# Optimization experiments

Measured on AMD Instinct MI355X. Metric: run time of the kernel, lower is better.

The kernel has to match this reference:

```python
import jax, jax.numpy as jnp
import numpy as np

VOCAB = 49408
D = 768
H = 12
DH = D // H
FF = 3072
L = 4
B = 32
S = 512
EPS = 1e-6


def _pos_encoding(seq_len, d):
    pos = np.arange(seq_len, dtype=np.float64)[:, None]
    j = np.arange(d, dtype=np.float64)[None, :]
    ang = pos / np.power(10000.0, 2.0 * (j // 2) / d)
    pe = np.where((np.arange(d) % 2) == 0, np.sin(ang), np.cos(ang))
    return jnp.asarray(pe, dtype=jnp.float32)  # [seq_len, d]


def _layernorm(x, g, b):
    m = jnp.mean(x, axis=-1, keepdims=True)
    v = jnp.mean(jnp.square(x - m), axis=-1, keepdims=True)
    return g * (x - m) * jax.lax.rsqrt(v + EPS) + b


def setup_inputs() -> dict:
    key = jax.random.key(0)
    ks = jax.random.split(key, 16)
    s = 0.02
    inp = {
        "tokens": jax.random.randint(ks[0], (B, S), 0, VOCAB, dtype=jnp.int32),
        "emb": jax.random.normal(ks[1], (VOCAB, D), jnp.float32) * s,
        "wq": jax.random.normal(ks[2], (L, D, D), jnp.float32) * s,
        "bq": jnp.zeros((L, D), jnp.float32),
        "wk": jax.random.normal(ks[3], (L, D, D), jnp.float32) * s,
        "bk": jnp.zeros((L, D), jnp.float32),
        "wv": jax.random.normal(ks[4], (L, D, D), jnp.float32) * s,
        "bv": jnp.zeros((L, D), jnp.float32),
        "wo": jax.random.normal(ks[5], (L, D, D), jnp.float32) * s,
        "bo": jnp.zeros((L, D), jnp.float32),
        "w1": jax.random.normal(ks[6], (L, D, FF), jnp.float32) * s,
        "b1": jnp.zeros((L, FF), jnp.float32),
        "w2": jax.random.normal(ks[7], (L, FF, D), jnp.float32) * s,
        "b2": jnp.zeros((L, D), jnp.float32),
        "ln1_g": jnp.ones((L, D), jnp.float32),
        "ln1_b": jnp.zeros((L, D), jnp.float32),
        "ln2_g": jnp.ones((L, D), jnp.float32),
        "ln2_b": jnp.zeros((L, D), jnp.float32),
        "wl": jax.random.normal(ks[8], (D, 32), jnp.float32) * s,
        "bl": jnp.zeros((32,), jnp.float32),
        "wout": jax.random.normal(ks[9], (32, 1), jnp.float32) * s,
        "bout": jnp.zeros((1,), jnp.float32),
    }
    return inp


def reference(tokens, emb, wq, bq, wk, bk, wv, bv, wo, bo, w1, b1, w2, b2,
              ln1_g, ln1_b, ln2_g, ln2_b, wl, bl, wout, bout):
    seq_len = tokens.shape[1]
    pe = _pos_encoding(seq_len, D)  # [S, D] constant
    x = emb[tokens] * jnp.sqrt(jnp.float32(D)) + pe[None, :, :]  # [B,S,D]
    scale = 1.0 / jnp.sqrt(jnp.float32(DH))
    for i in range(L):
        # multi-head attention (naive full score matrix, mask=None)
        q = (jnp.einsum('bsd,de->bse', x, wq[i]) + bq[i]).reshape(-1, seq_len, H, DH)
        k = (jnp.einsum('bsd,de->bse', x, wk[i]) + bk[i]).reshape(-1, seq_len, H, DH)
        v = (jnp.einsum('bsd,de->bse', x, wv[i]) + bv[i]).reshape(-1, seq_len, H, DH)
        scores = jnp.einsum('bqhd,bkhd->bhqk', q, k) * scale  # [B,H,S,S]
        attn = jax.nn.softmax(scores, axis=-1)
        av = jnp.einsum('bhqk,bkhd->bqhd', attn, v).reshape(-1, seq_len, D)
        attn_out = jnp.einsum('bsd,de->bse', av, wo[i]) + bo[i]
        out1 = _layernorm(x + attn_out, ln1_g[i], ln1_b[i])
        # FFN: relu -> dense
        h = jax.nn.relu(jnp.einsum('bsd,df->bsf', out1, w1[i]) + b1[i])
        ffn = jnp.einsum('bsf,fd->bsd', h, w2[i]) + b2[i]
        x = _layernorm(out1 + ffn, ln2_g[i], ln2_b[i])
    pooled = jnp.mean(x, axis=1)  # GlobalAveragePooling1D -> [B,D]
    h = jax.nn.gelu(pooled @ wl + bl, approximate=False)
    out = jax.nn.sigmoid(h @ wout + bout)  # [B,1]
    return out
```

## Files before the change

kernel.cpp:

```cpp
#include <hip/hip_runtime.h>
#include <hip/hip_bf16.h>
#include <math.h>


#define B_  32
#define S_  512
#define D_  768
#define H_  12
#define DH_ 64
#define FF_ 3072
#define L_  4
#define QKVSTR 2304

typedef __attribute__((ext_vector_type(8))) short short8;
typedef __attribute__((ext_vector_type(4))) short short4v;
typedef __attribute__((ext_vector_type(4))) float f32x4;

__device__ __forceinline__ void async16(const void* g, void* l) {
    __builtin_amdgcn_global_load_lds(
        (const __attribute__((address_space(1))) void*)g,
        (__attribute__((address_space(3))) void*)l, 16, 0, 0);
}

__device__ __forceinline__ ushort f2bf(float f) {
    __hip_bfloat16 h = __float2bfloat16(f);
    return __builtin_bit_cast(ushort, h);
}
__device__ __forceinline__ float bflo(uint u) { return __uint_as_float(u << 16); }
__device__ __forceinline__ float bfhi(uint u) { return __uint_as_float(u & 0xffff0000u); }

__device__ __forceinline__ short8 scale8_eighth(short8 v) {
    short8 r;
#pragma unroll
    for (int e = 0; e < 8; e++) {
        ushort u = (ushort)v[e];
        ushort ex = u & 0x7f80;
        r[e] = (short)(ex > 0x0180 ? (ushort)(u - 0x0180) : (ushort)(u & 0x8000));
    }
    return r;
}

__global__ void pe_kernel(float* __restrict__ pe) {
    int idx = blockIdx.x * 256 + threadIdx.x;
    if (idx >= S_ * D_) return;
    int s = idx / D_, j = idx % D_;
    double e = (2.0 * (double)(j >> 1)) / (double)D_;
    double denom = pow(10000.0, e);
    double ang = (double)s / denom;
    pe[idx] = (j & 1) ? (float)cos(ang) : (float)sin(ang);
}

__global__ void embed_kernel(const int* __restrict__ tokens,
                             const float* __restrict__ emb,
                             const float* __restrict__ pe,
                             __hip_bfloat16* __restrict__ xb) {
    int row = blockIdx.x;
    int s = row & (S_ - 1);
    int tok = tokens[row];
    float scale = sqrtf((float)D_);
    for (int i = threadIdx.x; i < D_; i += 256) {
        float v = emb[(size_t)tok * D_ + i] * scale + pe[s * D_ + i];
        xb[(size_t)row * D_ + i] = __float2bfloat16(v);
    }
}

__global__ __launch_bounds__(256) void transpose_bf16_l(
    const float* __restrict__ in, __hip_bfloat16* __restrict__ out,
    int R, int C, size_t inL, size_t outL)
{
    __shared__ float tile[32][33];
    in  += (size_t)blockIdx.z * inL;
    out += (size_t)blockIdx.z * outL;
    int tx = threadIdx.x & 31, ty = threadIdx.x >> 5;
    int c0 = blockIdx.x * 32, r0 = blockIdx.y * 32;
#pragma unroll
    for (int d = 0; d < 32; d += 8)
        tile[ty + d][tx] = in[(size_t)(r0 + ty + d) * C + c0 + tx];
    __syncthreads();
#pragma unroll
    for (int d = 0; d < 32; d += 8)
        out[(size_t)(c0 + ty + d) * R + r0 + tx] = __float2bfloat16(tile[tx][ty + d]);
}

__global__ void biascat(const float* __restrict__ bq, const float* __restrict__ bk,
                        const float* __restrict__ bv, float* __restrict__ o) {
    int i = blockIdx.x * 256 + threadIdx.x;
    int ll = i / QKVSTR, j = i % QKVSTR;
    o[i] = j < 768 ? bq[ll * 768 + j]
         : j < 1536 ? bk[ll * 768 + j - 768]
                    : bv[ll * 768 + j - 1536];
}

#define BAR()   __builtin_amdgcn_s_barrier()
#define LGKM0() asm volatile("s_waitcnt lgkmcnt(0)" ::: "memory")
#define VM4()   asm volatile("s_waitcnt vmcnt(4)" ::: "memory")
#define VM0()   asm volatile("s_waitcnt vmcnt(0)" ::: "memory")

#define STAGE_A(buf, h, kt) do { \
    async16(aSrc[h][0] + (kt) * 64, &lds[(buf) * 2][dOff[h][0]]); \
    async16(aSrc[h][1] + (kt) * 64, &lds[(buf) * 2][dOff[h][1]]); } while (0)
#define STAGE_B(buf, h, kt) do { \
    async16(bSrc[h][0] + (kt) * 64, &lds[(buf) * 2 + 1][dOff[h][0]]); \
    async16(bSrc[h][1] + (kt) * 64, &lds[(buf) * 2 + 1][dOff[h][1]]); } while (0)

#define LDA(buf, m, ks) (*(const short8*)((const char*)(&lds[(buf) * 2][0]) + \
    (size_t)((arow + (m) * 16) * 128 + cswz[ks])))
#define LDB(buf, n, ks) (*(const short8*)((const char*)(&lds[(buf) * 2 + 1][0]) + \
    (size_t)((brow + (n) * 16) * 128 + cswz[ks])))

#define MFMA_Q(mh, nh) do { \
    __builtin_amdgcn_s_setprio(1); \
    _Pragma("unroll") \
    for (int ks_ = 0; ks_ < 2; ks_++) { \
      _Pragma("unroll") \
      for (int n_ = 0; n_ < 2; n_++) { \
        _Pragma("unroll") \
        for (int m_ = 0; m_ < 4; m_++) { \
          acc[(mh) * 4 + m_][(nh) * 2 + n_] = \
              __builtin_amdgcn_mfma_f32_16x16x32_bf16( \
                  a[m_][ks_], b[(nh) * 2 + n_][ks_], \
                  acc[(mh) * 4 + m_][(nh) * 2 + n_], 0, 0, 0); \
        } } } \
    __builtin_amdgcn_s_setprio(0); \
} while (0)

template<int RELU>
__global__ __launch_bounds__(512, 2) void gemm256(
    const ushort* __restrict__ A,
    const ushort* __restrict__ Bt,
    const float* __restrict__ bias,
    __hip_bfloat16* __restrict__ C,
    int M, int N, int K, int NX)
{
    __shared__ alignas(16) ushort lds[4][16384];

    int t = threadIdx.x;
    int l = t & 63, w = t >> 6;
    int wmi = w >> 2, wni = w & 3;
    int lm = l & 15, lo = l >> 4;

    int nwg = gridDim.x;
    int bid = blockIdx.x;
    int lid = (nwg & 7) ? bid : ((bid & 7) * (nwg >> 3) + (bid >> 3));
    int bn = lid % NX, bm = lid / NX;
    int row0 = bm << 8, col0 = bn << 8;

    const ushort* aSrc[2][2];
    const ushort* bSrc[2][2];
    int dOff[2][2];
#pragma unroll
    for (int h = 0; h < 2; h++) {
#pragma unroll
        for (int c = 0; c < 2; c++) {
            int p = h * 16384 + c * 8192 + t * 16;
            int prow = p >> 7;
            int scolb = (p & 127) ^ ((prow & 7) << 4);
            dOff[h][c] = p >> 1;
            aSrc[h][c] = A  + (size_t)(row0 + prow) * K + (scolb >> 1);
            bSrc[h][c] = Bt + (size_t)(col0 + prow) * K + (scolb >> 1);
        }
    }

    int arow = wmi * 128 + lm;
    int brow = wni * 64 + lm;
    int swz = (lm & 7) << 4;
    int cswz[2];
    cswz[0] = (lo * 16) ^ swz;
    cswz[1] = (64 + lo * 16) ^ swz;

    f32x4 acc[8][4];
#pragma unroll
    for (int i = 0; i < 8; i++)
#pragma unroll
        for (int j = 0; j < 4; j++) acc[i][j] = (f32x4){0.f, 0.f, 0.f, 0.f};
    short8 a[4][2], b[4][2];

    const int NK = K >> 6;
    const int NI = NK >> 1;

    STAGE_A(0, 0, 0); STAGE_A(0, 1, 0);
    STAGE_B(0, 0, 0); STAGE_B(0, 1, 0);
    STAGE_B(1, 0, 1); STAGE_B(1, 1, 1);
    VM4();
    BAR();

    for (int i = 0; i < NI; i++) {
        int kt  = 2 * i;
        int ktA = (kt + 2 <= NK - 2) ? kt + 2 : NK - 2;
        int ktB = (kt + 3 <= NK - 1) ? kt + 3 : NK - 1;

#pragma unroll
        for (int m = 0; m < 4; m++) { a[m][0] = LDA(0, m, 0); a[m][1] = LDA(0, m, 1); }
#pragma unroll
        for (int n = 0; n < 2; n++) { b[n][0] = LDB(0, n, 0); b[n][1] = LDB(0, n, 1); }
        STAGE_A(1, 0, kt + 1);
        BAR(); LGKM0();
        MFMA_Q(0, 0);
        BAR();

#pragma unroll
        for (int n = 0; n < 2; n++) { b[2 + n][0] = LDB(0, 2 + n, 0); b[2 + n][1] = LDB(0, 2 + n, 1); }
        STAGE_A(1, 1, kt + 1);
        BAR(); LGKM0();
        MFMA_Q(0, 1);
        BAR();

#pragma unroll
        for (int m = 0; m < 4; m++) { a[m][0] = LDA(0, 4 + m, 0); a[m][1] = LDA(0, 4 + m, 1); }
        STAGE_B(0, 0, ktA);
        BAR(); LGKM0();
        MFMA_Q(1, 0);
        BAR();

        STAGE_B(0, 1, ktA);
        BAR(); LGKM0();
        MFMA_Q(1, 1);
        VM4();
        BAR();

#pragma unroll
        for (int m = 0; m < 4; m++) { a[m][0] = LDA(1, m, 0); a[m][1] = LDA(1, m, 1); }
#pragma unroll
        for (int n = 0; n < 2; n++) { b[n][0] = LDB(1, n, 0); b[n][1] = LDB(1, n, 1); }
        STAGE_A(0, 0, ktA);
        BAR(); LGKM0();
        MFMA_Q(0, 0);
        BAR();

#pragma unroll
        for (int n = 0; n < 2; n++) { b[2 + n][0] = LDB(1, 2 + n, 0); b[2 + n][1] = LDB(1, 2 + n, 1); }
        STAGE_A(0, 1, ktA);
        BAR(); LGKM0();
        MFMA_Q(0, 1);
        BAR();

#pragma unroll
        for (int m = 0; m < 4; m++) { a[m][0] = LDA(1, 4 + m, 0); a[m][1] = LDA(1, 4 + m, 1); }
        STAGE_B(1, 0, ktB);
        BAR(); LGKM0();
        MFMA_Q(1, 0);
        BAR();

        STAGE_B(1, 1, ktB);
        BAR(); LGKM0();
        MFMA_Q(1, 1);
        VM4();
        BAR();
    }

    VM0();
    BAR();

    ushort* eL = &lds[0][0];
    {
        int crow = wmi * 128;
        int ccol = wni * 64;
#pragma unroll
        for (int n = 0; n < 4; n++) {
            int c = ccol + n * 16 + lm;
            float bs = bias[col0 + c];
#pragma unroll
            for (int m = 0; m < 8; m++) {
#pragma unroll
                for (int r = 0; r < 4; r++) {
                    float v = acc[m][n][r] + bs;
                    if (RELU) v = fmaxf(v, 0.f);
                    int row = crow + m * 16 + lo * 4 + r;
                    int sc = c ^ (((lo * 4 + r) & 7) << 3);
                    eL[row * 256 + sc] = f2bf(v);
                }
            }
        }
    }
    __syncthreads();
    {
        int rsw = ((t >> 5) & 7) << 3;
#pragma unroll
        for (int i = 0; i < 16; i++) {
            int byteoff = i * 8192 + t * 16;
            int rr = byteoff >> 9;
            int cc = (byteoff & 511) >> 1;
            uint4 v = *(const uint4*)(eL + rr * 256 + (cc ^ rsw));
            *(uint4*)(C + (size_t)(row0 + rr) * N + col0 + cc) = v;
        }
    }
    (void)M;
}

#define PSTR 72
__global__ __launch_bounds__(256) void attn_mfma(
    const ushort* __restrict__ qkv,
    __hip_bfloat16* __restrict__ av)
{
    __shared__ alignas(16) ushort sQP[128 * PSTR];
    __shared__ alignas(16) ushort sK[64 * PSTR];
    __shared__ alignas(16) ushort sVt[64 * PSTR];

    int t = threadIdx.x;
    int qt = blockIdx.x, h = blockIdx.y, b = blockIdx.z;
    int w = t >> 6, l = t & 63;
    int lm = l & 15, lq = l >> 4;
    int wm = w * 32;

    const ushort* qbase = qkv + (size_t)(b * S_ + qt * 128) * QKVSTR + h * DH_;
    const ushort* kbase = qkv + (size_t)b * S_ * QKVSTR + 768 + h * DH_;
    const ushort* vbase = qkv + (size_t)b * S_ * QKVSTR + 1536 + h * DH_;

    {
        int r = t >> 1, c0 = (t & 1) * 32;
        const ushort* src = qbase + (size_t)r * QKVSTR + c0;
        ushort* dst = &sQP[r * PSTR + c0];
        *(uint4*)(dst + 0)  = *(const uint4*)(src + 0);
        *(uint4*)(dst + 8)  = *(const uint4*)(src + 8);
        *(uint4*)(dst + 16) = *(const uint4*)(src + 16);
        *(uint4*)(dst + 24) = *(const uint4*)(src + 24);
    }
    __syncthreads();
    short8 qf[2][2];
#pragma unroll
    for (int i = 0; i < 2; i++)
#pragma unroll
        for (int ks = 0; ks < 2; ks++)
            qf[i][ks] = scale8_eighth(
                *(const short8*)&sQP[(wm + i * 16 + lm) * PSTR + ks * 32 + lq * 8]);

    ushort* sPw = &sQP[(size_t)wm * PSTR];

    f32x4 accO[4][2];
    float mrun[2], lrun[2];
#pragma unroll
    for (int dk = 0; dk < 4; dk++)
#pragma unroll
        for (int i = 0; i < 2; i++) accO[dk][i] = (f32x4){0.f, 0.f, 0.f, 0.f};
    mrun[0] = mrun[1] = -1e30f;
    lrun[0] = lrun[1] = 0.f;

    for (int kt = 0; kt < S_ / 64; kt++) {
        __syncthreads();
        {
            int r = t >> 2, c0 = (t & 3) * 16;
            const ushort* ksrc = kbase + (size_t)(kt * 64 + r) * QKVSTR + c0;
            ushort* kdst = &sK[r * PSTR + c0];
            *(uint4*)(kdst + 0) = *(const uint4*)(ksrc + 0);
            *(uint4*)(kdst + 8) = *(const uint4*)(ksrc + 8);
            int p = t & 31, d0 = (t >> 5) * 8;
            const ushort* vsrc = vbase + (size_t)(kt * 64 + 2 * p) * QKVSTR + d0;
            uint4 v0 = *(const uint4*)(vsrc);
            uint4 v1 = *(const uint4*)(vsrc + QKVSTR);
            const ushort* e0 = (const ushort*)&v0;
            const ushort* e1 = (const ushort*)&v1;
#pragma unroll
            for (int j = 0; j < 8; j++) {
                uint pk = (uint)e0[j] | ((uint)e1[j] << 16);
                *(uint*)&sVt[(d0 + j) * PSTR + 2 * p] = pk;
            }
        }
        __syncthreads();

        f32x4 accS[4][2];
#pragma unroll
        for (int sb = 0; sb < 4; sb++)
#pragma unroll
            for (int i = 0; i < 2; i++) accS[sb][i] = (f32x4){0.f, 0.f, 0.f, 0.f};
#pragma unroll
        for (int ks = 0; ks < 2; ks++) {
#pragma unroll
            for (int sb = 0; sb < 4; sb++) {
                short8 kf = *(const short8*)&sK[(sb * 16 + lm) * PSTR + ks * 32 + lq * 8];
#pragma unroll
                for (int i = 0; i < 2; i++)
                    accS[sb][i] = __builtin_amdgcn_mfma_f32_16x16x32_bf16(
                        kf, qf[i][ks], accS[sb][i], 0, 0, 0);
            }
        }

        float pmax[2];
#pragma unroll
        for (int i = 0; i < 2; i++) {
            float m0 = accS[0][i][0];
#pragma unroll
            for (int sb = 0; sb < 4; sb++)
#pragma unroll
                for (int r = 0; r < 4; r++) m0 = fmaxf(m0, accS[sb][i][r]);
            m0 = fmaxf(m0, __shfl_xor(m0, 16));
            m0 = fmaxf(m0, __shfl_xor(m0, 32));
            pmax[i] = m0;
        }
        float alpha[2];
#pragma unroll
        for (int i = 0; i < 2; i++) {
            float mn = fmaxf(mrun[i], pmax[i]);
            alpha[i] = __expf(mrun[i] - mn);
            mrun[i] = mn;
        }
        float rsum[2] = {0.f, 0.f};
#pragma unroll
        for (int sb = 0; sb < 4; sb++)
#pragma unroll
            for (int i = 0; i < 2; i++)
#pragma unroll
                for (int r = 0; r < 4; r++) {
                    float p = __expf(accS[sb][i][r] - mrun[i]);
                    accS[sb][i][r] = p;
                    rsum[i] += p;
                }
#pragma unroll
        for (int i = 0; i < 2; i++) {
            rsum[i] += __shfl_xor(rsum[i], 16);
            rsum[i] += __shfl_xor(rsum[i], 32);
            lrun[i] = lrun[i] * alpha[i] + rsum[i];
        }

#pragma unroll
        for (int dk = 0; dk < 4; dk++)
#pragma unroll
            for (int i = 0; i < 2; i++)
#pragma unroll
                for (int r = 0; r < 4; r++) accO[dk][i][r] *= alpha[i];

#pragma unroll
        for (int i = 0; i < 2; i++)
#pragma unroll
            for (int sb = 0; sb < 4; sb++) {
                short4v pk;
#pragma unroll
                for (int r = 0; r < 4; r++) pk[r] = (short)f2bf(accS[sb][i][r]);
                *(short4v*)&sPw[(i * 16 + lm) * PSTR + sb * 16 + lq * 4] = pk;
            }

#pragma unroll
        for (int ks = 0; ks < 2; ks++) {
            short8 pf[2];
#pragma unroll
            for (int i = 0; i < 2; i++)
                pf[i] = *(const short8*)&sPw[(i * 16 + lm) * PSTR + ks * 32 + lq * 8];
#pragma unroll
            for (int dk = 0; dk < 4; dk++) {
                short8 vf = *(const short8*)&sVt[(dk * 16 + lm) * PSTR + ks * 32 + lq * 8];
#pragma unroll
                for (int i = 0; i < 2; i++)
                    accO[dk][i] = __builtin_amdgcn_mfma_f32_16x16x32_bf16(
                        vf, pf[i], accO[dk][i], 0, 0, 0);
            }
        }
    }

    float invl[2];
    invl[0] = 1.0f / lrun[0];
    invl[1] = 1.0f / lrun[1];
#pragma unroll
    for (int i = 0; i < 2; i++) {
        int row = qt * 128 + wm + i * 16 + lm;
        __hip_bfloat16* dst = av + (size_t)(b * S_ + row) * D_ + h * DH_;
#pragma unroll
        for (int dk = 0; dk < 4; dk++) {
            short4v ok;
#pragma unroll
            for (int r = 0; r < 4; r++) ok[r] = (short)f2bf(accO[dk][i][r] * invl[i]);
            *(short4v*)(dst + dk * 16 + lq * 4) = ok;
        }
    }
}

__global__ __launch_bounds__(256) void add_ln(
    __hip_bfloat16* __restrict__ xb,
    const __hip_bfloat16* __restrict__ r, const float* __restrict__ g,
    const float* __restrict__ bta)
{
    __shared__ float sred[256];
    int row = blockIdx.x, t = threadIdx.x;
    uint* xu = (uint*)(xb + (size_t)row * D_);
    const uint* ru = (const uint*)(r + (size_t)row * D_);
    uint ux0 = xu[t], ur0 = ru[t];
    float a0 = bflo(ux0) + bflo(ur0);
    float a1 = bfhi(ux0) + bfhi(ur0);
    float a2 = 0.f, a3 = 0.f;
    if (t < 128) {
        uint ux1 = xu[256 + t], ur1 = ru[256 + t];
        a2 = bflo(ux1) + bflo(ur1);
        a3 = bfhi(ux1) + bfhi(ur1);
    }
    sred[t] = a0 + a1 + a2 + a3;
    __syncthreads();
    for (int o = 128; o > 0; o >>= 1) { if (t < o) sred[t] += sred[t + o]; __syncthreads(); }
    float mean = sred[0] * (1.0f / D_);
    __syncthreads();
    float d0 = a0 - mean, d1 = a1 - mean;
    float d2 = a2 - mean, d3 = a3 - mean;
    sred[t] = d0 * d0 + d1 * d1 + (t < 128 ? d2 * d2 + d3 * d3 : 0.f);
    __syncthreads();
    for (int o = 128; o > 0; o >>= 1) { if (t < o) sred[t] += sred[t + o]; __syncthreads(); }
    float rstd = rsqrtf(sred[0] * (1.0f / D_) + 1e-6f);
    {
        float2 gv = ((const float2*)g)[t];
        float2 bv = ((const float2*)bta)[t];
        float o0 = gv.x * d0 * rstd + bv.x;
        float o1 = gv.y * d1 * rstd + bv.y;
        xu[t] = (uint)f2bf(o0) | ((uint)f2bf(o1) << 16);
    }
    if (t < 128) {
        float2 gv = ((const float2*)g)[256 + t];
        float2 bv = ((const float2*)bta)[256 + t];
        float o2 = gv.x * d2 * rstd + bv.x;
        float o3 = gv.y * d3 * rstd + bv.y;
        xu[256 + t] = (uint)f2bf(o2) | ((uint)f2bf(o3) << 16);
    }
}

__global__ void pool_kernel(const __hip_bfloat16* __restrict__ xb,
                            float* __restrict__ pooled) {
    int idx = blockIdx.x * 256 + threadIdx.x;
    int b = idx / D_, d = idx % D_;
    float acc = 0.f;
    const __hip_bfloat16* p = xb + (size_t)b * S_ * D_ + d;
    for (int s = 0; s < S_; s++) acc += __bfloat162float(p[(size_t)s * D_]);
    pooled[idx] = acc * (1.0f / S_);
}

__global__ void head_kernel(const float* __restrict__ pooled,
                            const float* __restrict__ wl,
                            const float* __restrict__ bl,
                            const float* __restrict__ wout,
                            const float* __restrict__ bout,
                            float* __restrict__ out)
{
    __shared__ float hb[32];
    int b = blockIdx.x, t = threadIdx.x;
    if (t < 32) {
        float z = bl[t];
        for (int d = 0; d < D_; d++) z += pooled[b * D_ + d] * wl[d * 32 + t];
        hb[t] = 0.5f * z * (1.0f + erff(z * 0.70710678118654752f));
    }
    __syncthreads();
    if (t == 0) {
        float z = bout[0];
        for (int j = 0; j < 32; j++) z += hb[j] * wout[j];
        out[b] = 1.0f / (1.0f + expf(-z));
    }
}

extern "C" void kernel_launch(void* const* d_in, const int* in_sizes, int n_in,
                              void* d_out, int out_size, void* d_ws, size_t ws_size,
                              hipStream_t stream)
{
    (void)in_sizes; (void)n_in; (void)out_size; (void)ws_size;
    const int*   tokens = (const int*)  d_in[0];
    const float* emb    = (const float*)d_in[1];
    const float* wq     = (const float*)d_in[2];
    const float* bq     = (const float*)d_in[3];
    const float* wk     = (const float*)d_in[4];
    const float* bk     = (const float*)d_in[5];
    const float* wv     = (const float*)d_in[6];
    const float* bv     = (const float*)d_in[7];
    const float* wo     = (const float*)d_in[8];
    const float* bo     = (const float*)d_in[9];
    const float* w1     = (const float*)d_in[10];
    const float* b1     = (const float*)d_in[11];
    const float* w2     = (const float*)d_in[12];
    const float* b2     = (const float*)d_in[13];
    const float* ln1g   = (const float*)d_in[14];
    const float* ln1b   = (const float*)d_in[15];
    const float* ln2g   = (const float*)d_in[16];
    const float* ln2b   = (const float*)d_in[17];
    const float* wl     = (const float*)d_in[18];
    const float* bl     = (const float*)d_in[19];
    const float* wout   = (const float*)d_in[20];
    const float* bout   = (const float*)d_in[21];
    float* out = (float*)d_out;

    char* ws = (char*)d_ws;
    size_t off = 0;
    auto alloc = [&](size_t n) -> void* {
        char* p = ws + off;
        off = (off + n + 255) & ~(size_t)255;
        return (void*)p;
    };
    const size_t XBYTES = (size_t)B_ * S_ * D_ * 4;
    const size_t XBF    = XBYTES / 2;
    float*          pe     = (float*)alloc((size_t)S_ * D_ * 4);
    __hip_bfloat16* xb     = (__hip_bfloat16*)alloc(XBF);
    __hip_bfloat16* r_bf   = (__hip_bfloat16*)alloc(XBF);
    char*           arena  = (char*)alloc(4 * XBF);
    __hip_bfloat16* qkv_bf = (__hip_bfloat16*)arena;
    __hip_bfloat16* av_bf  = (__hip_bfloat16*)(arena + 3 * XBF);
    __hip_bfloat16* h_bf   = (__hip_bfloat16*)arena;
    __hip_bfloat16* wT     = (__hip_bfloat16*)alloc((size_t)L_ * 7077888 * 2);
    float*          qkvbias= (float*)alloc((size_t)L_ * QKVSTR * 4);
    float*          pooled = (float*)alloc((size_t)B_ * D_ * 4);

    const int M = B_ * S_;
    const size_t DD = (size_t)D_ * D_;
    const size_t DF = (size_t)D_ * FF_;
    const size_t LSTRIDE = 4 * DD + 2 * DF;

    transpose_bf16_l<<<dim3(D_ / 32, D_ / 32, L_), 256, 0, stream>>>(
        wq, wT + 0 * DD, D_, D_, DD, LSTRIDE);
    transpose_bf16_l<<<dim3(D_ / 32, D_ / 32, L_), 256, 0, stream>>>(
        wk, wT + 1 * DD, D_, D_, DD, LSTRIDE);
    transpose_bf16_l<<<dim3(D_ / 32, D_ / 32, L_), 256, 0, stream>>>(
        wv, wT + 2 * DD, D_, D_, DD, LSTRIDE);
    transpose_bf16_l<<<dim3(D_ / 32, D_ / 32, L_), 256, 0, stream>>>(
        wo, wT + 3 * DD, D_, D_, DD, LSTRIDE);
    transpose_bf16_l<<<dim3(FF_ / 32, D_ / 32, L_), 256, 0, stream>>>(
        w1, wT + 4 * DD, D_, FF_, DF, LSTRIDE);
    transpose_bf16_l<<<dim3(D_ / 32, FF_ / 32, L_), 256, 0, stream>>>(
        w2, wT + 4 * DD + DF, FF_, D_, DF, LSTRIDE);
    biascat<<<(L_ * QKVSTR) / 256, 256, 0, stream>>>(bq, bk, bv, qkvbias);

    pe_kernel<<<(S_ * D_ + 255) / 256, 256, 0, stream>>>(pe);
    embed_kernel<<<M, 256, 0, stream>>>(tokens, emb, pe, xb);

    for (int l = 0; l < L_; l++) {
        __hip_bfloat16* wl_base = wT + (size_t)l * LSTRIDE;
        const ushort* qkvT = (const ushort*)(wl_base + 0 * DD);
        const ushort* woT  = (const ushort*)(wl_base + 3 * DD);
        const ushort* w1T  = (const ushort*)(wl_base + 4 * DD);
        const ushort* w2T  = (const ushort*)(wl_base + 4 * DD + DF);

        gemm256<0><<<dim3((QKVSTR / 256) * (M / 256)), 512, 0, stream>>>(
            (const ushort*)xb, qkvT, qkvbias + (size_t)l * QKVSTR, qkv_bf,
            M, QKVSTR, D_, QKVSTR / 256);

        attn_mfma<<<dim3(S_ / 128, H_, B_), 256, 0, stream>>>(
            (const ushort*)qkv_bf, av_bf);

        gemm256<0><<<dim3((D_ / 256) * (M / 256)), 512, 0, stream>>>(
            (const ushort*)av_bf, woT, bo + l * D_, r_bf, M, D_, D_, D_ / 256);
        add_ln<<<M, 256, 0, stream>>>(xb, r_bf, ln1g + l * D_, ln1b + l * D_);

        gemm256<1><<<dim3((FF_ / 256) * (M / 256)), 512, 0, stream>>>(
            (const ushort*)xb, w1T, b1 + l * FF_, h_bf, M, FF_, D_, FF_ / 256);
        gemm256<0><<<dim3((D_ / 256) * (M / 256)), 512, 0, stream>>>(
            (const ushort*)h_bf, w2T, b2 + l * D_, r_bf, M, D_, FF_, D_ / 256);
        add_ln<<<M, 256, 0, stream>>>(xb, r_bf, ln2g + l * D_, ln2b + l * D_);
    }

    pool_kernel<<<(B_ * D_) / 256, 256, 0, stream>>>(xb, pooled);
    head_kernel<<<B_, 64, 0, stream>>>(pooled, wl, bl, wout, bout, out);
}
```

Before: 1.886 ms.

## Register-prefetch next K/V tile and skip softmax rescale when max stable

The attention kernel now loads the next K/V tile from global memory into registers while the current tile is being computed, using two alternating register buffers and an unroll-by-two loop, so load latency overlaps the MFMA and softmax work. It also adds a lazy rescale: the running max and the output accumulator are only updated when some lane's new max exceeds the old by more than 8, which avoids the per-tile alpha multiply and exp. The prefetch costs extra registers, which may reduce occupancy. The lazy rescale lets exponentials reach up to e^8 before normalisation; this is safe in fp32 but slightly changes the bf16 P values.

```diff
diff --git a/kernel.cpp b/kernel.cpp
--- a/kernel.cpp
+++ b/kernel.cpp
@@ -306,6 +306,12 @@
     const ushort* kbase = qkv + (size_t)b * S_ * QKVSTR + 768 + h * DH_;
     const ushort* vbase = qkv + (size_t)b * S_ * QKVSTR + 1536 + h * DH_;
 
+    int kr = t >> 2, kc0 = (t & 3) * 16;
+    int vp = t & 31, vd0 = (t >> 5) * 8;
+    const ushort* kptr = kbase + (size_t)kr * QKVSTR + kc0;
+    const ushort* vptr = vbase + (size_t)(2 * vp) * QKVSTR + vd0;
+    const size_t KTS = (size_t)64 * QKVSTR;
+
     {
         int r = t >> 1, c0 = (t & 1) * 32;
         const ushort* src = qbase + (size_t)r * QKVSTR + c0;
@@ -315,6 +321,12 @@
         *(uint4*)(dst + 16) = *(const uint4*)(src + 16);
         *(uint4*)(dst + 24) = *(const uint4*)(src + 24);
     }
+    uint4 kA0 = *(const uint4*)(kptr);
+    uint4 kA1 = *(const uint4*)(kptr + 8);
+    uint4 vA0 = *(const uint4*)(vptr);
+    uint4 vA1 = *(const uint4*)(vptr + QKVSTR);
+    uint4 kB0, kB1, vB0, vB1;
+
     __syncthreads();
     short8 qf[2][2];
 #pragma unroll
@@ -335,28 +347,20 @@
     mrun[0] = mrun[1] = -1e30f;
     lrun[0] = lrun[1] = 0.f;
 
-    for (int kt = 0; kt < S_ / 64; kt++) {
-        __syncthreads();
-        {
-            int r = t >> 2, c0 = (t & 3) * 16;
-            const ushort* ksrc = kbase + (size_t)(kt * 64 + r) * QKVSTR + c0;
-            ushort* kdst = &sK[r * PSTR + c0];
-            *(uint4*)(kdst + 0) = *(const uint4*)(ksrc + 0);
-            *(uint4*)(kdst + 8) = *(const uint4*)(ksrc + 8);
-            int p = t & 31, d0 = (t >> 5) * 8;
-            const ushort* vsrc = vbase + (size_t)(kt * 64 + 2 * p) * QKVSTR + d0;
-            uint4 v0 = *(const uint4*)(vsrc);
-            uint4 v1 = *(const uint4*)(vsrc + QKVSTR);
-            const ushort* e0 = (const ushort*)&v0;
-            const ushort* e1 = (const ushort*)&v1;
-#pragma unroll
-            for (int j = 0; j < 8; j++) {
-                uint pk = (uint)e0[j] | ((uint)e1[j] << 16);
-                *(uint*)&sVt[(d0 + j) * PSTR + 2 * p] = pk;
-            }
-        }
-        __syncthreads();
-
+    auto stage_write = [&](const uint4& k0, const uint4& k1,
+                           const uint4& v0, const uint4& v1) {
+        *(uint4*)&sK[kr * PSTR + kc0]     = k0;
+        *(uint4*)&sK[kr * PSTR + kc0 + 8] = k1;
+        const ushort* e0 = (const ushort*)&v0;
+        const ushort* e1 = (const ushort*)&v1;
+#pragma unroll
+        for (int jj = 0; jj < 8; jj++) {
+            uint pk = (uint)e0[jj] | ((uint)e1[jj] << 16);
+            *(uint*)&sVt[(vd0 + jj) * PSTR + 2 * vp] = pk;
+        }
+    };
+
+    auto compute = [&]() {
         f32x4 accS[4][2];
 #pragma unroll
         for (int sb = 0; sb < 4; sb++)
@@ -386,12 +390,18 @@
             m0 = fmaxf(m0, __shfl_xor(m0, 32));
             pmax[i] = m0;
         }
-        float alpha[2];
 #pragma unroll
         for (int i = 0; i < 2; i++) {
-            float mn = fmaxf(mrun[i], pmax[i]);
-            alpha[i] = __expf(mrun[i] - mn);
-            mrun[i] = mn;
+            if (!__all(pmax[i] - mrun[i] <= 8.0f)) {
+                float mn = fmaxf(mrun[i], pmax[i]);
+                float al = __expf(mrun[i] - mn);
+                mrun[i] = mn;
+                lrun[i] *= al;
+#pragma unroll
+                for (int dk = 0; dk < 4; dk++)
+#pragma unroll
+                    for (int r = 0; r < 4; r++) accO[dk][i][r] *= al;
+            }
         }
         float rsum[2] = {0.f, 0.f};
 #pragma unroll
@@ -408,15 +418,8 @@
         for (int i = 0; i < 2; i++) {
             rsum[i] += __shfl_xor(rsum[i], 16);
             rsum[i] += __shfl_xor(rsum[i], 32);
-            lrun[i] = lrun[i] * alpha[i] + rsum[i];
-        }
-
-#pragma unroll
-        for (int dk = 0; dk < 4; dk++)
-#pragma unroll
-            for (int i = 0; i < 2; i++)
-#pragma unroll
-                for (int r = 0; r < 4; r++) accO[dk][i][r] *= alpha[i];
+            lrun[i] += rsum[i];
+        }
 
 #pragma unroll
         for (int i = 0; i < 2; i++)
@@ -443,6 +446,34 @@
                         vf, pf[i], accO[dk][i], 0, 0, 0);
             }
         }
+    };
+
+    for (int j = 0; j < S_ / 128; j++) {
+        __syncthreads();
+        stage_write(kA0, kA1, vA0, vA1);
+        {
+            const ushort* kp = kptr + (size_t)(2 * j + 1) * KTS;
+            const ushort* vq = vptr + (size_t)(2 * j + 1) * KTS;
+            kB0 = *(const uint4*)(kp);
+            kB1 = *(const uint4*)(kp + 8);
+            vB0 = *(const uint4*)(vq);
+            vB1 = *(const uint4*)(vq + QKVSTR);
+        }
+        __syncthreads();
+        compute();
+
+        __syncthreads();
+        stage_write(kB0, kB1, vB0, vB1);
+        if (j < S_ / 128 - 1) {
+            const ushort* kp = kptr + (size_t)(2 * j + 2) * KTS;
+            const ushort* vq = vptr + (size_t)(2 * j + 2) * KTS;
+            kA0 = *(const uint4*)(kp);
+            kA1 = *(const uint4*)(kp + 8);
+            vA0 = *(const uint4*)(vq);
+            vA1 = *(const uint4*)(vq + QKVSTR);
+        }
+        __syncthreads();
+        compute();
     }
 
     float invl[2];
```

Measured after the change: 1.766 ms. -6.3%, faster.
